# Optimization experiments

Hardware: AMD Instinct MI355X
Metric: run time of the kernel (lower is better)

Reference implementation:

```python
import jax, jax.numpy as jnp
import numpy as np

B, V, S = 128, 64, 40
D, H, VOC = 256, 256, 20000


def setup_inputs() -> dict:
    key = jax.random.key(0)
    ks = jax.random.split(key, 26)
    g = lambda k, shp: (jax.random.normal(k, shp, dtype=jnp.float32) * 0.02)
    inp = {}
    inp['input_seqs'] = jax.random.randint(ks[0], (B, V, S), 0, VOC + 1)
    inp['mask'] = jnp.zeros((B, V), jnp.float32)
    inp['length'] = jax.random.randint(ks[1], (B,), 1, V + 1)
    inp['seq_time_step'] = jax.random.uniform(ks[2], (B, V), dtype=jnp.float32)
    inp['codemask'] = jnp.zeros((B, V, S), jnp.float32)
    inp['label'] = jax.random.randint(ks[3], (B,), 0, 2)
    # embedding table; padding_idx=-1 in torch == row VOC zeroed
    inp['emb'] = g(ks[4], (VOC + 1, D)).at[VOC].set(0.0)
    # LSTM (single layer, batch_first): torch gate order i,f,g,o
    inp['W_ih'] = g(ks[5], (4 * H, D))
    inp['W_hh'] = g(ks[6], (4 * H, H))
    inp['b_ih'] = g(ks[7], (4 * H,))
    inp['b_hh'] = g(ks[8], (4 * H,))
    # attention projections
    inp['Whk'] = g(ks[9], (D, H))
    inp['bhk'] = g(ks[10], (D,))
    inp['W1'] = g(ks[11], (64, 2 * H))
    inp['b1'] = g(ks[12], (64,))
    inp['W2'] = g(ks[13], (2, 64))
    inp['b2'] = g(ks[14], (2,))
    # classifyer MLP: d -> 4d -> 2d -> 2
    inp['C1W'] = g(ks[15], (4 * D, D))
    inp['C1b'] = g(ks[16], (4 * D,))
    inp['C2W'] = g(ks[17], (2 * D, 4 * D))
    inp['C2b'] = g(ks[18], (2 * D,))
    inp['CoW'] = g(ks[19], (2, 2 * D))
    inp['Cob'] = g(ks[20], (2,))
    return inp


def _lstm(x, W_ih, W_hh, b_ih, b_hh):
    # x: [B,T,D] -> hs: [B,T,H]; torch gate order i,f,g,o
    Bsz = x.shape[0]
    Hd = W_hh.shape[1]
    xg = jnp.einsum('btd,gd->btg', x, W_ih) + b_ih + b_hh  # [B,T,4H]

    def step(carry, xg_t):
        h, c = carry
        gates = xg_t + h @ W_hh.T
        i, f, gg, o = jnp.split(gates, 4, axis=-1)
        i = jax.nn.sigmoid(i); f = jax.nn.sigmoid(f)
        gg = jnp.tanh(gg); o = jax.nn.sigmoid(o)
        c = f * c + i * gg
        h = o * jnp.tanh(c)
        return (h, c), h

    z = jnp.zeros((Bsz, Hd), x.dtype)
    _, hs = jax.lax.scan(step, (z, z), jnp.swapaxes(xg, 0, 1))
    return jnp.swapaxes(hs, 0, 1)


def _classify(h, C1W, C1b, C2W, C2b, CoW, Cob):
    h = jax.nn.relu(h @ C1W.T + C1b)
    h = jax.nn.relu(h @ C2W.T + C2b)
    return h @ CoW.T + Cob


def reference(input_seqs, mask, length, seq_time_step, codemask, label,
              emb, W_ih, W_hh, b_ih, b_hh, Whk, bhk, W1, b1, W2, b2,
              C1W, C1b, C2W, C2b, CoW, Cob):
    # before(): embedding gather -> relu -> sum over codes (eval mode, no dropout)
    v = jax.nn.relu(emb[input_seqs]).sum(-2)  # [B,V,D]
    h = _lstm(v, W_ih, W_hh, b_ih, b_hh)       # [B,V,H]

    # vectorized form of the per-timestep attention loop:
    # bar_v[:,0]=v[:,0]; for i>=1: mix of e_k=v[:,0] and w_hk(h[:,i-1])
    e_k = v[:, :1, :]                                   # [B,1,D]
    wh = h @ Whk.T + bhk                                # [B,V,D]
    wh_prev = wh[:, :-1, :]                             # [B,V-1,D] (h at i-1)
    e_b = jnp.broadcast_to(e_k, wh_prev.shape)
    cat = jnp.concatenate([e_b, wh_prev], axis=-1)      # [B,V-1,2D]
    attn = jax.nn.softmax(jnp.tanh(cat @ W1.T + b1) @ W2.T + b2, axis=-1)
    bar_rest = e_b * attn[..., 0:1] + wh_prev * attn[..., 1:2]
    bar_v = jnp.concatenate([v[:, :1, :], bar_rest], axis=1)  # [B,V,D]

    # GAN stand-in (external injected module): identity
    Dec_V, Gen_V = bar_v, bar_v
    gen_h = _lstm(Gen_V, W_ih, W_hh, b_ih, b_hh)

    og = _classify(h, C1W, C1b, C2W, C2b, CoW, Cob)        # [B,V,2]
    fake = _classify(gen_h, C1W, C1b, C2W, C2b, CoW, Cob)  # [B,V,2]
    final_og = og[:, -1, :]
    final_fake = fake[:, -1, :]
    return (final_og, final_fake, Dec_V, Gen_V, seq_time_step, label)
```

## Files before the change

kernel.cpp:

```cpp
#include <hip/hip_runtime.h>

#define DEV __device__ __forceinline__

typedef float f32x4 __attribute__((ext_vector_type(4)));
typedef short s16x8 __attribute__((ext_vector_type(8)));
typedef short s16x4 __attribute__((ext_vector_type(4)));

DEV unsigned short f2bf(float f){
  unsigned int u = __float_as_uint(f);
  u += 0x7fffu + ((u>>16)&1u);
  return (unsigned short)(u>>16);
}
DEV float bf2f(unsigned short h){ return __uint_as_float(((unsigned int)h)<<16); }

#if __has_builtin(__builtin_amdgcn_rcpf)
DEV float frcp_(float x){ return __builtin_amdgcn_rcpf(x); }
#else
DEV float frcp_(float x){ return 1.f/x; }
#endif
#if __has_builtin(__builtin_amdgcn_exp2f)
DEV float fexp2_(float x){ return __builtin_amdgcn_exp2f(x); }
#else
DEV float fexp2_(float x){ return exp2f(x); }
#endif

DEV float tanh_(float x){
  x = fminf(x, 30.f);
  float e = fexp2_(2.8853900817779268f*x);
  return (e-1.f)*frcp_(e+1.f);
}

DEV unsigned char f2e4m3(float x){
  unsigned int u = __float_as_uint(x);
  unsigned int s = (u>>24)&0x80u;
  unsigned int mag = u & 0x7fffffffu;
  if (mag > 0x43E00000u) mag = 0x43E00000u;
  mag += 0x000FFFFFu + ((mag>>20)&1u);
  int e = (int)(mag>>23) - 120;
  unsigned int m = (mag>>20)&7u;
  unsigned int r = (e<=0) ? 0u : (((unsigned)e<<3)|m);
  return (unsigned char)(s|r);
}

DEV f32x4 mfma_bf16(s16x8 a, s16x8 b, f32x4 c){
  return __builtin_amdgcn_mfma_f32_16x16x32_bf16(a,b,c,0,0,0);
}
DEV f32x4 mfma_fp8(long a, long b, f32x4 c){
  return __builtin_amdgcn_mfma_f32_16x16x32_fp8_fp8(a,b,c,0,0,0);
}

DEV void lds_barrier(){
  asm volatile("s_waitcnt lgkmcnt(0)\n\ts_barrier" ::: "memory");
}

DEV unsigned aload_rlx(unsigned* p){
  return __hip_atomic_load(p, __ATOMIC_RELAXED, __HIP_MEMORY_SCOPE_AGENT);
}
DEV void astore_rlx(unsigned* p, unsigned v){
  __hip_atomic_store(p, v, __ATOMIC_RELAXED, __HIP_MEMORY_SCOPE_AGENT);
}
DEV void aadd_rlx(unsigned* p, unsigned v){
  __hip_atomic_fetch_add(p, v, __ATOMIC_RELAXED, __HIP_MEMORY_SCOPE_AGENT);
}
DEV void acq_fence(){ __builtin_amdgcn_fence(__ATOMIC_ACQUIRE, "agent"); }
DEV void spin_rlx(unsigned* p, unsigned tgt){
  while (aload_rlx(p) < tgt) __builtin_amdgcn_s_sleep(2);
  asm volatile("" ::: "memory");
}
DEV void block_wait(unsigned* p, unsigned tgt){
  if (threadIdx.x == 0) spin_rlx(p, tgt);
  __syncthreads();
}
DEV void block_wait_acq(unsigned* p, unsigned tgt){
  if (threadIdx.x == 0){ spin_rlx(p, tgt); acq_fence(); }
  __syncthreads();
}
DEV s16x4 aload64(const unsigned short* p){
  unsigned long long v = __hip_atomic_load((unsigned long long*)(void*)p,
      __ATOMIC_RELAXED, __HIP_MEMORY_SCOPE_AGENT);
  union { unsigned long long u; s16x4 s; } c; c.u = v; return c.s;
}
DEV void astore64(unsigned short* p, s16x4 v){
  union { s16x4 s; unsigned long long u; } c; c.s = v;
  __hip_atomic_store((unsigned long long*)(void*)p, c.u,
      __ATOMIC_RELAXED, __HIP_MEMORY_SCOPE_AGENT);
}
DEV s16x8 aload128(const unsigned short* p){
  s16x4 a = aload64(p), b = aload64(p+4);
  s16x8 r;
  r[0]=a[0]; r[1]=a[1]; r[2]=a[2]; r[3]=a[3];
  r[4]=b[0]; r[5]=b[1]; r[6]=b[2]; r[7]=b[3];
  return r;
}
DEV float aloadf(const float* p){
  return __hip_atomic_load((float*)(void*)p, __ATOMIC_RELAXED, __HIP_MEMORY_SCOPE_AGENT);
}
DEV void astoref(float* p, float v){
  __hip_atomic_store(p, v, __ATOMIC_RELAXED, __HIP_MEMORY_SCOPE_AGENT);
}
DEV void astore16(unsigned short* p, unsigned short v){
  __hip_atomic_store(p, v, __ATOMIC_RELAXED, __HIP_MEMORY_SCOPE_AGENT);
}
DEV void vm_drain(){ asm volatile("s_waitcnt vmcnt(0)" ::: "memory"); }
DEV void ntf(float* p, float v){ __builtin_nontemporal_store(v, p); }

#define Bx 128
#define Vx 64
#define Sx 40
#define Dx 256
#define Hx 256
#define NVOC 20001

#define OFF_OG   0
#define OFF_FAKE 256
#define OFF_DECV 512
#define OFF_GENV 2097664
#define OFF_STS  4194816
#define OFF_LBL  4203008

#define PW_IH  0
#define PW_HH  262144
#define PW_HK  524288
#define PW_1   589824
#define PC_1   622592
#define PC_2   884736
#define PC_O   1409024
#define P_TOT  1410048

#define HPB 264
#define BFP 272
#define WHP 272

#define FCT(t)  ((t)*32)
#define FXG(t)  (2048 + (t)*32)
#define FUC     4096
#define FXG1(t) (4352 + (t)*32)
#define XDONE   6528
#define Y1D     6656
#define Y2D     6784
#define XG1A    6912
#define FTOT    8192

__global__ void k_cvt(const float* __restrict__ emb, unsigned short* __restrict__ emb16,
                      const float* __restrict__ W_ih, const float* __restrict__ Whh,
                      const float* __restrict__ Whk, const float* __restrict__ W1,
                      const float* __restrict__ C1W, const float* __restrict__ C2W,
                      const float* __restrict__ CoW,
                      unsigned short* __restrict__ pool, unsigned char* __restrict__ whh8,
                      const float* __restrict__ sts, const int* __restrict__ label,
                      float* __restrict__ out, unsigned* __restrict__ flags){
  int bx = blockIdx.x, tid = threadIdx.x;
  if (bx < NVOC){
    size_t i = (size_t)bx*256 + tid;
    emb16[i] = f2bf(emb[i]);
    return;
  }
  if (bx < NVOC + 6532){
    int i = (bx - NVOC)*256 + tid;
    if (i < P_TOT){
      float v;
      if      (i < PW_HH) v = W_ih[i - PW_IH];
      else if (i < PW_HK) v = Whh [i - PW_HH];
      else if (i < PW_1 ) v = Whk [i - PW_HK];
      else if (i < PC_1 ) v = W1  [i - PW_1 ];
      else if (i < PC_2 ) v = C1W [i - PC_1 ];
      else if (i < PC_O ) v = C2W [i - PC_2 ];
      else                v = CoW [i - PC_O ];
      pool[i] = f2bf(v);
    } else {
      whh8[i - P_TOT] = f2e4m3(16.f*Whh[i - P_TOT]);
    }
    return;
  }
  for (int i=tid;i<FTOT;i+=256) flags[i] = 0u;
  for (int i=tid;i<Bx*Vx;i+=256) out[OFF_STS + i] = sts[i];
  if (tid < Bx) out[OFF_LBL + tid] = (float)label[tid];
}

__global__ void k_pre2(const int* __restrict__ seqs, const unsigned short* __restrict__ emb16,
                       unsigned short* __restrict__ v16,
                       float* __restrict__ decv, float* __restrict__ genv){
  int bt = blockIdx.x, d = threadIdx.x;
  const int* sp = seqs + (size_t)bt*Sx;
  float acc = 0.f;
  #pragma unroll 8
  for (int s=0;s<Sx;s++) acc += fmaxf(bf2f(emb16[(size_t)sp[s]*Dx + d]), 0.f);
  size_t o = (size_t)bt*Dx + d;
  v16[o] = f2bf(acc);
  if ((bt & 63) == 0){ decv[o] = acc; genv[o] = acc; }
}

DEV void lstm_act(const f32x4* A, float* cst, float* hv){
  const float K1 = 1.4426950408889634f/256.f;
  #pragma unroll
  for (int r=0;r<4;r++){
    float iv = frcp_(1.f + fexp2_(-K1*A[0][r]));
    float fv = frcp_(1.f + fexp2_(-K1*A[1][r]));
    float eg = fexp2_(2.f*K1*A[2][r]);
    float gv = (eg-1.f)*frcp_(eg+1.f);
    float ov = frcp_(1.f + fexp2_(-K1*A[3][r]));
    float cv = fv*cst[r] + iv*gv;
    cst[r] = cv;
    float ec = fexp2_(2.8853900817779268f*fminf(cv,30.f));
    hv[r] = ov*(ec-1.f)*frcp_(ec+1.f);
  }
}

DEV void store_h_fp8(unsigned char* hn, int q, const float* hv){
#if __has_builtin(__builtin_amdgcn_cvt_pk_fp8_f32)
  int p01 = __builtin_amdgcn_cvt_pk_fp8_f32(16.f*hv[0], 16.f*hv[1], 0, false);
  int p23 = __builtin_amdgcn_cvt_pk_fp8_f32(16.f*hv[2], 16.f*hv[3], 0, false);
  hn[(q*4+0)*HPB] = (unsigned char)p01;
  hn[(q*4+1)*HPB] = (unsigned char)(p01>>8);
  hn[(q*4+2)*HPB] = (unsigned char)p23;
  hn[(q*4+3)*HPB] = (unsigned char)(p23>>8);
#else
  #pragma unroll
  for (int r=0;r<4;r++) hn[(q*4+r)*HPB] = f2e4m3(16.f*hv[r]);
#endif
}

DEV void scan1_body(unsigned char* smem, const unsigned char* __restrict__ W8,
                    const unsigned short* __restrict__ xg1, unsigned short* __restrict__ hist,
                    int g, unsigned* __restrict__ flags){
  unsigned char*  hl  = smem;
  unsigned short* h1b = (unsigned short*)(smem + 8448);
  int tid = threadIdx.x;
  int w = tid>>6, l = tid&63, lm = l&15, q = l>>4;
  int j = w*16 + lm;
  for (int i=tid;i<8448;i+=1024) hl[i] = 0;
  long Bf[4][8];
  #pragma unroll
  for (int qq=0;qq<4;qq++){
    int n = qq*256 + j;
    #pragma unroll
    for (int kk=0;kk<8;kk++)
      Bf[qq][kk] = *(const long*)(W8 + (size_t)n*256 + kk*32 + q*8);
  }
  float cst[4] = {0.f,0.f,0.f,0.f};
  const unsigned short* xgb = xg1 + (size_t)g*16384 + q*4;
  s16x4 xc[4], xn[4];
  block_wait(&flags[FXG1(0)], 2);
  #pragma unroll
  for (int qq=0;qq<4;qq++) xc[qq] = aload64(xgb + (qq*256+j)*16);
  int all1 = 0;
  const unsigned char* hrd = hl + lm*HPB + q*8;
  #pragma unroll 1
  for (int t=0;t<Vx;t++){
    if (t > 0){
      asm volatile("s_waitcnt vmcnt(0)" ::: "memory");
      __syncthreads();
    }
    if (tid == 0){
      if (t > 0) aadd_rlx(&flags[FCT(t-1)], 1);
      if (t < Vx-1 && !all1){
        spin_rlx(&flags[FXG1(t+1)], 2);
        all1 = (aload_rlx(&flags[XG1A]) >= 128);
      }
    }
    __syncthreads();
    if (t < Vx-1){
      #pragma unroll
      for (int qq=0;qq<4;qq++)
        xn[qq] = aload64(xgb + (size_t)(t+1)*131072 + (qq*256+j)*16);
    }
    const unsigned char* hb = hrd + (t&1)*4224;
    f32x4 A[4];
    #pragma unroll
    for (int qq=0;qq<4;qq++){
      #pragma unroll
      for (int r=0;r<4;r++) A[qq][r] = bf2f((unsigned short)xc[qq][r]);
    }
    #pragma unroll
    for (int kk=0;kk<8;kk++){
      long af = *(const long*)(hb + kk*32);
      A[0] = mfma_fp8(af, Bf[0][kk], A[0]);
      A[1] = mfma_fp8(af, Bf[1][kk], A[1]);
      A[2] = mfma_fp8(af, Bf[2][kk], A[2]);
      A[3] = mfma_fp8(af, Bf[3][kk], A[3]);
    }
    float hv[4];
    lstm_act(A, cst, hv);
    store_h_fp8(hl + ((t+1)&1)*4224 + j, q, hv);
    #pragma unroll
    for (int r=0;r<4;r++) h1b[(q*4+r)*BFP + j] = f2bf(hv[r]);
    lds_barrier();
    {
      int row = tid>>6, c4 = (tid&63)*4;
      s16x4 hx = *(const s16x4*)(h1b + row*BFP + c4);
      astore64(hist + ((size_t)t*Bx + g*16 + row)*Hx + c4, hx);
    }
    #pragma unroll
    for (int qq=0;qq<4;qq++) xc[qq] = xn[qq];
  }
  asm volatile("s_waitcnt vmcnt(0)" ::: "memory");
  __syncthreads();
  if (tid == 0){ aadd_rlx(&flags[FCT(63)], 1); aadd_rlx(&flags[XDONE], 1); }
}

DEV void scan2_body(unsigned char* smem, const unsigned char* __restrict__ W8,
                    const unsigned short* __restrict__ xg2, unsigned short* __restrict__ h2,
                    int g, unsigned* __restrict__ flags){
  unsigned char*  hl  = smem;
  unsigned short* h1b = (unsigned short*)(smem + 8448);
  int tid = threadIdx.x;
  int w = tid>>6, l = tid&63, lm = l&15, q = l>>4;
  int j = w*16 + lm;
  for (int i=tid;i<8448;i+=1024) hl[i] = 0;
  long Bf[4][8];
  #pragma unroll
  for (int qq=0;qq<4;qq++){
    int n = qq*256 + j;
    #pragma unroll
    for (int kk=0;kk<8;kk++)
      Bf[qq][kk] = *(const long*)(W8 + (size_t)n*256 + kk*32 + q*8);
  }
  float cst[4] = {0.f,0.f,0.f,0.f};
  const unsigned short* xgb = xg2 + (size_t)g*16384 + q*4;
  s16x4 xc[4], xn1[4], xn2[4];
  block_wait(&flags[FXG(0)], 1);
  #pragma unroll
  for (int qq=0;qq<4;qq++) xc[qq] = aload64(xgb + (qq*256+j)*16);
  block_wait(&flags[FXG(1)], 1);
  #pragma unroll
  for (int qq=0;qq<4;qq++) xn1[qq] = aload64(xgb + 131072 + (qq*256+j)*16);
  int skip = 0;
  const unsigned char* hrd = hl + lm*HPB + q*8;
  #pragma unroll 1
  for (int t=0;t<Vx;t++){
    if (t+2 < Vx){
      if (tid == 0){
        if (!skip) spin_rlx(&flags[FXG(t+2)], 1);
        skip = (t+3 < Vx) && (aload_rlx(&flags[FXG(t+3)]) >= 1);
      }
      __syncthreads();
      #pragma unroll
      for (int qq=0;qq<4;qq++)
        xn2[qq] = aload64(xgb + (size_t)(t+2)*131072 + (qq*256+j)*16);
    }
    const unsigned char* hb = hrd + (t&1)*4224;
    f32x4 A[4];
    #pragma unroll
    for (int qq=0;qq<4;qq++){
      #pragma unroll
      for (int r=0;r<4;r++) A[qq][r] = bf2f((unsigned short)xc[qq][r]);
    }
    #pragma unroll
    for (int kk=0;kk<8;kk++){
      long af = *(const long*)(hb + kk*32);
      A[0] = mfma_fp8(af, Bf[0][kk], A[0]);
      A[1] = mfma_fp8(af, Bf[1][kk], A[1]);
      A[2] = mfma_fp8(af, Bf[2][kk], A[2]);
      A[3] = mfma_fp8(af, Bf[3][kk], A[3]);
    }
    float hv[4];
    lstm_act(A, cst, hv);
    store_h_fp8(hl + ((t+1)&1)*4224 + j, q, hv);
    if (t == Vx-1){
      #pragma unroll
      for (int r=0;r<4;r++) h1b[(q*4+r)*BFP + j] = f2bf(hv[r]);
      lds_barrier();
      {
        int row = tid>>6, c4 = (tid&63)*4;
        s16x4 hx = *(const s16x4*)(h1b + row*BFP + c4);
        astore64(h2 + (size_t)(g*16 + row)*Hx + c4, hx);
      }
      asm volatile("s_waitcnt vmcnt(0)" ::: "memory");
      __syncthreads();
      if (tid == 0) aadd_rlx(&flags[XDONE], 1);
    } else {
      lds_barrier();
    }
    #pragma unroll
    for (int qq=0;qq<4;qq++){ xc[qq] = xn1[qq]; xn1[qq] = xn2[qq]; }
  }
}

template<int ALDS>
DEV void xg2_tile(const unsigned short* Ab, const unsigned short* __restrict__ pool,
                  const float* __restrict__ b_ih, const float* __restrict__ b_hh,
                  unsigned short* __restrict__ xg2, int tile, int w, int lm, int q){
  int mh = (w&1)*64, nb = (w>>1)*128;
  #pragma unroll 1
  for (int sc=0; sc<4; sc++){
    int n0 = nb + sc*32;
    f32x4 acc[4][2];
    #pragma unroll
    for (int nt=0;nt<2;nt++){
      int n = n0 + nt*16 + lm;
      float bz = b_ih[n] + b_hh[n];
      #pragma unroll
      for (int mt=0;mt<4;mt++) acc[mt][nt] = (f32x4){bz,bz,bz,bz};
    }
    #pragma unroll
    for (int kk=0;kk<8;kk++){
      s16x8 bfr[2];
      #pragma unroll
      for (int nt=0;nt<2;nt++){
        int n = n0 + nt*16 + lm;
        bfr[nt] = *(const s16x8*)(pool + PW_IH + (size_t)n*256 + kk*32 + q*8);
      }
      #pragma unroll
      for (int mt=0;mt<4;mt++){
        int row = mh + mt*16 + lm;
        s16x8 afr = ALDS ? *(const s16x8*)(Ab + (size_t)row*WHP + kk*32 + q*8)
                         : *(const s16x8*)(Ab + (size_t)row*Vx*Dx + kk*32 + q*8);
        acc[mt][0] = mfma_bf16(afr, bfr[0], acc[mt][0]);
        acc[mt][1] = mfma_bf16(afr, bfr[1], acc[mt][1]);
      }
    }
    #pragma unroll
    for (int mt=0;mt<4;mt++){
      int m = mh + mt*16 + q*4;
      int gg = m>>4;
      #pragma unroll
      for (int nt=0;nt<2;nt++){
        int n = n0 + nt*16 + lm;
        s16x4 sv;
        #pragma unroll
        for (int r=0;r<4;r++) sv[r] = (short)f2bf(256.f*acc[mt][nt][r]);
        astore64(xg2 + (((size_t)tile*8 + gg)*1024 + n)*16 + (m&15), sv);
      }
    }
  }
}

DEV void worker_body(unsigned short* whs, int t,
    const unsigned short* __restrict__ hist1, const unsigned short* __restrict__ v16,
    const float* __restrict__ u, const unsigned short* __restrict__ pool,
    const float* __restrict__ bhk, const float* __restrict__ W2, const float* __restrict__ b2,
    const float* __restrict__ b_ih, const float* __restrict__ b_hh,
    float* __restrict__ decv, float* __restrict__ genv,
    unsigned short* __restrict__ xg2, unsigned* __restrict__ flags){
  int tid = threadIdx.x, w = tid>>6, l = tid&63, lm = l&15, q = l>>4;
  if (t == 63){
    xg2_tile<0>(v16, pool, b_ih, b_hh, xg2, 0, w, lm, q);
    vm_drain();
    __syncthreads();
    if (tid == 0) astore_rlx(&flags[FXG(0)], 1);
    return;
  }
  block_wait(&flags[FCT(t)], 8);
  {
    int r0 = (w&7)*16, n0 = (w>>3)*128;
    const unsigned short* Ar = hist1 + ((size_t)t*Bx + r0 + lm)*Hx;
    f32x4 acc[8];
    #pragma unroll
    for (int nt=0;nt<8;nt++){
      float bz = bhk[n0 + nt*16 + lm];
      acc[nt] = (f32x4){bz,bz,bz,bz};
    }
    #pragma unroll
    for (int kk=0;kk<8;kk++){
      s16x8 afr = aload128(Ar + kk*32 + q*8);
      #pragma unroll
      for (int nt=0;nt<8;nt++){
        int n = n0 + nt*16 + lm;
        s16x8 bfr = *(const s16x8*)(pool + PW_HK + (size_t)n*256 + kk*32 + q*8);
        acc[nt] = mfma_bf16(afr, bfr, acc[nt]);
      }
    }
    #pragma unroll
    for (int nt=0;nt<8;nt++){
      int n = n0 + nt*16 + lm, mb = r0 + q*4;
      #pragma unroll
      for (int r=0;r<4;r++) whs[(size_t)(mb+r)*WHP + n] = f2bf(acc[nt][r]);
    }
  }
  if (tid == 0) spin_rlx(&flags[FUC], 8);
  __syncthreads();
  if (w < 8){
    int m0l = w*16;
    f32x4 a2[4];
    #pragma unroll
    for (int nt=0;nt<4;nt++){
      int n = nt*16 + lm;
      #pragma unroll
      for (int r=0;r<4;r++) a2[nt][r] = aloadf(u + (size_t)(m0l + q*4 + r)*64 + n);
    }
    #pragma unroll
    for (int kk=0;kk<8;kk++){
      s16x8 afr = *(const s16x8*)(whs + (size_t)(m0l+lm)*WHP + kk*32 + q*8);
      #pragma unroll
      for (int nt=0;nt<4;nt++){
        int n = nt*16 + lm;
        s16x8 bfr = *(const s16x8*)(pool + PW_1 + (size_t)n*512 + 256 + kk*32 + q*8);
        a2[nt] = mfma_bf16(afr, bfr, a2[nt]);
      }
    }
    float p0a[4] = {0,0,0,0}, p1a[4] = {0,0,0,0};
    #pragma unroll
    for (int nt=0;nt<4;nt++){
      int n = nt*16 + lm;
      float w2a = W2[n], w2b = W2[64+n];
      #pragma unroll
      for (int r=0;r<4;r++){
        float z = tanh_(a2[nt][r]);
        p0a[r] += z*w2a; p1a[r] += z*w2b;
      }
    }
    #pragma unroll
    for (int s=1;s<16;s<<=1){
      #pragma unroll
      for (int r=0;r<4;r++){ p0a[r] += __shfl_xor(p0a[r], s, 16); p1a[r] += __shfl_xor(p1a[r], s, 16); }
    }
    float bb0 = b2[0], bb1 = b2[1];
    int d0 = lm*16;
    #pragma unroll
    for (int r=0;r<4;r++){
      int b = m0l + q*4 + r;
      float g0 = p0a[r]+bb0, g1 = p1a[r]+bb1;
      float al0 = frcp_(1.f + fexp2_(1.4426950408889634f*(g1-g0)));
      float al1 = 1.f - al0;
      const unsigned short* ek = v16 + (size_t)b*Vx*Dx + d0;
      unsigned short* whp = whs + (size_t)b*WHP + d0;
      size_t ob = ((size_t)b*Vx + (t+1))*Dx + d0;
      #pragma unroll
      for (int c=0;c<2;c++){
        s16x8 e8 = *(const s16x8*)(ek + c*8);
        s16x8 w8 = *(const s16x8*)(whp + c*8);
        s16x8 o16;
        #pragma unroll
        for (int jj=0;jj<8;jj++){
          float o = al0*bf2f((unsigned short)e8[jj]) + al1*bf2f((unsigned short)w8[jj]);
          ntf(decv + ob + c*8 + jj, o);
          ntf(genv + ob + c*8 + jj, o);
          o16[jj] = (short)f2bf(o);
        }
        *(s16x8*)(whp + c*8) = o16;
      }
    }
  }
  __syncthreads();
  xg2_tile<1>(whs, pool, b_ih, b_hh, xg2, t+1, w, lm, q);
  vm_drain();
  __syncthreads();
  if (tid == 0) astore_rlx(&flags[FXG(t+1)], 1);
}

DEV void xg1_body(const unsigned short* __restrict__ v16, const unsigned short* __restrict__ pool,
                  const float* __restrict__ b_ih, const float* __restrict__ b_hh,
                  unsigned short* __restrict__ xg1, int blk, unsigned* __restrict__ flags){
  int tid = threadIdx.x, w = tid>>6, l = tid&63, lm = l&15, q = l>>4;
  int m0 = blk*64;
  int n0 = w*64;
  f32x4 acc[4][4];
  #pragma unroll
  for (int nt=0;nt<4;nt++){
    int n = n0 + nt*16 + lm;
    float bz = b_ih[n] + b_hh[n];
    #pragma unroll
    for (int mt=0;mt<4;mt++) acc[mt][nt] = (f32x4){bz,bz,bz,bz};
  }
  const s16x8* Arow[4];
  #pragma unroll
  for (int mt=0;mt<4;mt++){
    int m = m0 + mt*16 + lm;
    Arow[mt] = (const s16x8*)(v16 + ((size_t)(m&127)*Vx + (m>>7))*(size_t)Dx);
  }
  for (int kk=0; kk<8; kk++){
    s16x8 bfr[4];
    #pragma unroll
    for (int nt=0;nt<4;nt++){
      int n = n0 + nt*16 + lm;
      bfr[nt] = *(const s16x8*)(pool + PW_IH + (size_t)n*256 + kk*32 + q*8);
    }
    #pragma unroll
    for (int mt=0;mt<4;mt++){
      s16x8 afr = Arow[mt][kk*4 + q];
      #pragma unroll
      for (int nt=0;nt<4;nt++)
        acc[mt][nt] = mfma_bf16(afr, bfr[nt], acc[mt][nt]);
    }
  }
  #pragma unroll
  for (int mt=0;mt<4;mt++){
    int mbase = m0 + mt*16 + q*4;
    int tt = mbase>>7, bb = mbase&127;
    int gg = bb>>4;
    #pragma unroll
    for (int nt=0;nt<4;nt++){
      int n = n0 + nt*16 + lm;
      s16x4 sv;
      #pragma unroll
      for (int r=0;r<4;r++) sv[r] = (short)f2bf(256.f*acc[mt][nt][r]);
      astore64(xg1 + (((size_t)tt*8 + gg)*1024 + n)*16 + (bb&15), sv);
    }
  }
  vm_drain();
  __syncthreads();
  if (tid == 0){ aadd_rlx(&flags[FXG1(blk>>1)], 1); aadd_rlx(&flags[XG1A], 1); }
}

DEV void cls_gemm(const unsigned short* __restrict__ A, const unsigned short* __restrict__ Bw,
                  const float* __restrict__ bias, unsigned short* __restrict__ C,
                  int K, int Ntot, int bxx, int byy){
  int tid = threadIdx.x, w = tid>>6, l = tid&63, lm = l&15, q = l>>4;
  int m0 = bxx*64, n0 = byy*256 + w*64;
  f32x4 acc[4][4];
  #pragma unroll
  for (int nt=0;nt<4;nt++){
    int n = n0 + nt*16 + lm;
    float bz = bias[n];
    #pragma unroll
    for (int mt=0;mt<4;mt++) acc[mt][nt] = (f32x4){bz,bz,bz,bz};
  }
  const s16x8* Arow[4];
  #pragma unroll
  for (int mt=0;mt<4;mt++)
    Arow[mt] = (const s16x8*)(A + (size_t)(m0 + mt*16 + lm)*K);
  int kkn = K/32;
  for (int kk=0; kk<kkn; kk++){
    s16x8 bfr[4];
    #pragma unroll
    for (int nt=0;nt<4;nt++){
      int n = n0 + nt*16 + lm;
      bfr[nt] = *(const s16x8*)(Bw + (size_t)n*K + kk*32 + q*8);
    }
    #pragma unroll
    for (int mt=0;mt<4;mt++){
      s16x8 afr = Arow[mt][kk*4 + q];
      #pragma unroll
      for (int nt=0;nt<4;nt++)
        acc[mt][nt] = mfma_bf16(afr, bfr[nt], acc[mt][nt]);
    }
  }
  #pragma unroll
  for (int mt=0;mt<4;mt++){
    int mbase = m0 + mt*16 + q*4;
    #pragma unroll
    for (int nt=0;nt<4;nt++){
      int n = n0 + nt*16 + lm;
      #pragma unroll
      for (int r=0;r<4;r++)
        astore16(C + (size_t)(mbase+r)*Ntot + n, f2bf(fmaxf(acc[mt][nt][r], 0.f)));
    }
  }
}

__global__ __launch_bounds__(1024) void k_mega(
    const unsigned char* __restrict__ W8,
    unsigned short* __restrict__ xg1, unsigned short* __restrict__ xg2,
    unsigned short* __restrict__ hist1,
    const unsigned short* __restrict__ v16, float* __restrict__ u,
    const unsigned short* __restrict__ pool,
    const float* __restrict__ bhk, const float* __restrict__ W2, const float* __restrict__ b2,
    const float* __restrict__ b1, const float* __restrict__ b_ih, const float* __restrict__ b_hh,
    const float* __restrict__ C1b, const float* __restrict__ C2b, const float* __restrict__ Cob,
    float* __restrict__ decv, float* __restrict__ genv, float* __restrict__ out,
    unsigned* __restrict__ flags){
  __shared__ __align__(16) unsigned char smem[69632];
  int blk = blockIdx.x;
  unsigned short* X  = hist1 + (size_t)(Vx-1)*Bx*Hx;
  unsigned short* h2 = hist1 + (size_t)Vx*Bx*Hx;
  unsigned short* y1 = xg1;
  unsigned short* y2 = xg1 + 262144;
  if (blk < 8){
    scan1_body(smem, W8, xg1, hist1, blk, flags);
  } else if (blk < 16){
    scan2_body(smem, W8, xg2, h2, blk-8, flags);
  } else if (blk < 80){
    worker_body((unsigned short*)smem, blk-16, hist1, v16, u, pool, bhk, W2, b2,
                b_ih, b_hh, decv, genv, xg2, flags);
  } else if (blk < 88){
    int t2 = (blk-80)*1024 + threadIdx.x;
    int b = t2>>6, n = t2&63;
    const s16x8* vr = (const s16x8*)(v16 + (size_t)b*Vx*Dx);
    const s16x8* wr = (const s16x8*)(pool + PW_1 + (size_t)n*512);
    float a = b1[n];
    for (int kk=0;kk<32;kk++){
      s16x8 x = vr[kk], ww = wr[kk];
      #pragma unroll
      for (int jj=0;jj<8;jj++) a += bf2f((unsigned short)x[jj])*bf2f((unsigned short)ww[jj]);
    }
    astoref(u + t2, a);
    vm_drain();
    __syncthreads();
    if (threadIdx.x == 0) aadd_rlx(&flags[FUC], 1);
  } else if (blk < 216){
    xg1_body(v16, pool, b_ih, b_hh, xg1, blk-88, flags);
  } else if (blk < 232){
    block_wait_acq(&flags[XDONE], 16);
    int p = blk-216;
    if (threadIdx.x < 256) cls_gemm(X, pool+PC_1, C1b, y1, 256, 1024, p&3, p>>2);
    vm_drain();
    __syncthreads();
    if (threadIdx.x == 0) aadd_rlx(&flags[Y1D], 1);
  } else if (blk < 240){
    block_wait_acq(&flags[Y1D], 16);
    int p = blk-232;
    if (threadIdx.x < 256) cls_gemm(y1, pool+PC_2, C2b, y2, 1024, 512, p&3, p>>2);
    vm_drain();
    __syncthreads();
    if (threadIdx.x == 0) aadd_rlx(&flags[Y2D], 1);
  } else {
    block_wait_acq(&flags[Y2D], 8);
    if (threadIdx.x < 256){
      int t2 = (blk-240)*256 + threadIdx.x;
      int m = t2>>1, n = t2&1;
      const s16x8* yr = (const s16x8*)(y2 + (size_t)m*512);
      const s16x8* wr = (const s16x8*)(pool + PC_O + (size_t)n*512);
      float a = Cob[n];
      for (int kk=0;kk<64;kk++){
        s16x8 yv = yr[kk], ww = wr[kk];
        #pragma unroll
        for (int jj=0;jj<8;jj++) a += bf2f((unsigned short)yv[jj])*bf2f((unsigned short)ww[jj]);
      }
      int base = (m < 128) ? (OFF_OG + m*2) : (OFF_FAKE + (m-128)*2);
      out[base + n] = a;
    }
  }
}

extern "C" void kernel_launch(void* const* d_in, const int* in_sizes, int n_in,
                              void* d_out, int out_size, void* d_ws, size_t ws_size,
                              hipStream_t stream) {
  const int*   seqs  = (const int*)d_in[0];
  const float* sts   = (const float*)d_in[3];
  const int*   label = (const int*)d_in[5];
  const float* emb   = (const float*)d_in[6];
  const float* W_ih  = (const float*)d_in[7];
  const float* W_hh  = (const float*)d_in[8];
  const float* b_ih  = (const float*)d_in[9];
  const float* b_hh  = (const float*)d_in[10];
  const float* Whk   = (const float*)d_in[11];
  const float* bhk   = (const float*)d_in[12];
  const float* W1    = (const float*)d_in[13];
  const float* b1    = (const float*)d_in[14];
  const float* W2    = (const float*)d_in[15];
  const float* b2    = (const float*)d_in[16];
  const float* C1b   = (const float*)d_in[18];
  const float* C2b   = (const float*)d_in[20];
  const float* Cob   = (const float*)d_in[22];
  float* out = (float*)d_out;

  char* ws = (char*)d_ws;
  unsigned short* v16    = (unsigned short*)(ws + 0);
  unsigned short* xg1    = (unsigned short*)(ws + (4<<20));
  unsigned short* hist1  = (unsigned short*)(ws + (20<<20));
  unsigned short* xg2    = (unsigned short*)(ws + (25<<20));
  unsigned short* emb16  = xg2;
  float*          u      = (float*)(ws + (41<<20));
  unsigned char*  whh8   = (unsigned char*)(ws + (41<<20) + (64<<10));
  unsigned*       flags  = (unsigned*)(ws + (41<<20) + (384<<10));
  unsigned short* pool   = (unsigned short*)(ws + (42<<20));

  float* decv = out + OFF_DECV;
  float* genv = out + OFF_GENV;

  k_cvt<<<dim3(NVOC + 6532 + 1), dim3(256), 0, stream>>>(emb, emb16,
      W_ih, W_hh, Whk, W1, (const float*)d_in[17], (const float*)d_in[19],
      (const float*)d_in[21], pool, whh8, sts, label, out, flags);
  k_pre2<<<dim3(8192), dim3(256), 0, stream>>>(seqs, emb16, v16, decv, genv);
  k_mega<<<dim3(242), dim3(1024), 0, stream>>>(whh8, xg1, xg2, hist1, v16, u, pool,
      bhk, W2, b2, b1, b_ih, b_hh, C1b, C2b, Cob, decv, genv, out, flags);
}
```

Before: 508.9 us.

## Move input-gate GEMM to separate kernel and batch LSTM step flag signaling

The input-to-gate projection for the first LSTM now runs as its own kernel before the persistent mega-kernel, instead of as extra blocks inside it guarded by per-timestep flags. That lets the scan read xg1 with plain loads and no spin-waits. The scan now signals downstream consumers only every four timesteps, with a cheap LDS barrier in between. Conversion work is also regrouped into two kernels. The trade-off is an extra launch, losing the overlap between the GEMM and the scan, and coarser producer/consumer granularity for the workers that wait on FCT flags.

```diff
diff --git a/kernel.cpp b/kernel.cpp
--- a/kernel.cpp
+++ b/kernel.cpp
@@ -85,16 +85,6 @@
   __hip_atomic_store((unsigned long long*)(void*)p, c.u,
       __ATOMIC_RELAXED, __HIP_MEMORY_SCOPE_AGENT);
 }
-DEV s16x8 aload128(const unsigned short* p){
-  s16x4 a = aload64(p), b = aload64(p+4);
-  s16x8 r;
-  r[0]=a[0]; r[1]=a[1]; r[2]=a[2]; r[3]=a[3];
-  r[4]=b[0]; r[5]=b[1]; r[6]=b[2]; r[7]=b[3];
-  return r;
-}
-DEV float aloadf(const float* p){
-  return __hip_atomic_load((float*)(void*)p, __ATOMIC_RELAXED, __HIP_MEMORY_SCOPE_AGENT);
-}
 DEV void astoref(float* p, float v){
   __hip_atomic_store(p, v, __ATOMIC_RELAXED, __HIP_MEMORY_SCOPE_AGENT);
 }
@@ -134,14 +124,19 @@
 #define FCT(t)  ((t)*32)
 #define FXG(t)  (2048 + (t)*32)
 #define FUC     4096
-#define FXG1(t) (4352 + (t)*32)
-#define XDONE   6528
-#define Y1D     6656
-#define Y2D     6784
-#define XG1A    6912
+#define XDONE   4224
+#define Y1D     4352
+#define Y2D     4480
 #define FTOT    8192
 
-__global__ void k_cvt(const float* __restrict__ emb, unsigned short* __restrict__ emb16,
+__global__ void k_cvt_emb(const float* __restrict__ emb, unsigned short* __restrict__ emb16){
+  size_t i = (size_t)blockIdx.x*256 + threadIdx.x;
+  emb16[i] = f2bf(emb[i]);
+}
+
+__global__ void k_pre(const int* __restrict__ seqs, const unsigned short* __restrict__ emb16,
+                      unsigned short* __restrict__ v16,
+                      float* __restrict__ decv, float* __restrict__ genv,
                       const float* __restrict__ W_ih, const float* __restrict__ Whh,
                       const float* __restrict__ Whk, const float* __restrict__ W1,
                       const float* __restrict__ C1W, const float* __restrict__ C2W,
@@ -150,13 +145,19 @@
                       const float* __restrict__ sts, const int* __restrict__ label,
                       float* __restrict__ out, unsigned* __restrict__ flags){
   int bx = blockIdx.x, tid = threadIdx.x;
-  if (bx < NVOC){
-    size_t i = (size_t)bx*256 + tid;
-    emb16[i] = f2bf(emb[i]);
+  if (bx < 8192){
+    int bt = bx, d = tid;
+    const int* sp = seqs + (size_t)bt*Sx;
+    float acc = 0.f;
+    #pragma unroll 8
+    for (int s=0;s<Sx;s++) acc += fmaxf(bf2f(emb16[(size_t)sp[s]*Dx + d]), 0.f);
+    size_t o = (size_t)bt*Dx + d;
+    v16[o] = f2bf(acc);
+    if ((bt & 63) == 0){ decv[o] = acc; genv[o] = acc; }
     return;
   }
-  if (bx < NVOC + 6532){
-    int i = (bx - NVOC)*256 + tid;
+  if (bx < 14724){
+    int i = (bx-8192)*256 + tid;
     if (i < P_TOT){
       float v;
       if      (i < PW_HH) v = W_ih[i - PW_IH];
@@ -167,7 +168,7 @@
       else if (i < PC_O ) v = C2W [i - PC_2 ];
       else                v = CoW [i - PC_O ];
       pool[i] = f2bf(v);
-    } else {
+    } else if (i < P_TOT + 262144){
       whh8[i - P_TOT] = f2e4m3(16.f*Whh[i - P_TOT]);
     }
     return;
@@ -177,17 +178,68 @@
   if (tid < Bx) out[OFF_LBL + tid] = (float)label[tid];
 }
 
-__global__ void k_pre2(const int* __restrict__ seqs, const unsigned short* __restrict__ emb16,
-                       unsigned short* __restrict__ v16,
-                       float* __restrict__ decv, float* __restrict__ genv){
-  int bt = blockIdx.x, d = threadIdx.x;
-  const int* sp = seqs + (size_t)bt*Sx;
-  float acc = 0.f;
-  #pragma unroll 8
-  for (int s=0;s<Sx;s++) acc += fmaxf(bf2f(emb16[(size_t)sp[s]*Dx + d]), 0.f);
-  size_t o = (size_t)bt*Dx + d;
-  v16[o] = f2bf(acc);
-  if ((bt & 63) == 0){ decv[o] = acc; genv[o] = acc; }
+template<int MODE_A, int MODE_C, int RELU>
+__global__ void k_gemm(const unsigned short* __restrict__ A, const unsigned short* __restrict__ Bw,
+                       const float* __restrict__ bias1, const float* __restrict__ bias2,
+                       unsigned short* __restrict__ C, int K, int Ntot, float scale){
+  int tid = threadIdx.x, w = tid>>6, l = tid&63, lm = l&15, q = l>>4;
+  int m0 = blockIdx.x*64;
+  int n0 = blockIdx.y*256 + w*64;
+  f32x4 acc[4][4];
+  #pragma unroll
+  for (int nt=0;nt<4;nt++){
+    int n = n0 + nt*16 + lm;
+    float bz = bias1 ? bias1[n] : 0.f;
+    if (bias2) bz += bias2[n];
+    #pragma unroll
+    for (int mt=0;mt<4;mt++) acc[mt][nt] = (f32x4){bz,bz,bz,bz};
+  }
+  const s16x8* Arow[4];
+  #pragma unroll
+  for (int mt=0;mt<4;mt++){
+    int m = m0 + mt*16 + lm;
+    size_t off = (MODE_A==0) ? (size_t)m*K : ((size_t)(m&127)*Vx + (m>>7))*(size_t)K;
+    Arow[mt] = (const s16x8*)(A + off);
+  }
+  int kkn = K/32;
+  for (int kk=0; kk<kkn; kk++){
+    s16x8 bfr[4];
+    #pragma unroll
+    for (int nt=0;nt<4;nt++){
+      int n = n0 + nt*16 + lm;
+      bfr[nt] = *(const s16x8*)(Bw + (size_t)n*K + kk*32 + q*8);
+    }
+    #pragma unroll
+    for (int mt=0;mt<4;mt++){
+      s16x8 afr = Arow[mt][kk*4 + q];
+      #pragma unroll
+      for (int nt=0;nt<4;nt++)
+        acc[mt][nt] = mfma_bf16(afr, bfr[nt], acc[mt][nt]);
+    }
+  }
+  #pragma unroll
+  for (int mt=0;mt<4;mt++){
+    int mbase = m0 + mt*16 + q*4;
+    #pragma unroll
+    for (int nt=0;nt<4;nt++){
+      int n = n0 + nt*16 + lm;
+      if (MODE_C==0){
+        #pragma unroll
+        for (int r=0;r<4;r++){
+          float val = scale*acc[mt][nt][r];
+          if (RELU) val = fmaxf(val, 0.f);
+          C[(size_t)(mbase+r)*Ntot + n] = f2bf(val);
+        }
+      } else {
+        int tt = mbase>>7, bb = mbase&127;
+        int gg = bb>>4;
+        s16x4 sv;
+        #pragma unroll
+        for (int r=0;r<4;r++) sv[r] = (short)f2bf(scale*acc[mt][nt][r]);
+        *(s16x4*)(C + (((size_t)tt*8 + gg)*1024 + n)*16 + (bb&15)) = sv;
+      }
+    }
+  }
 }
 
 DEV void lstm_act(const f32x4* A, float* cst, float* hv){
@@ -240,29 +292,16 @@
   float cst[4] = {0.f,0.f,0.f,0.f};
   const unsigned short* xgb = xg1 + (size_t)g*16384 + q*4;
   s16x4 xc[4], xn[4];
-  block_wait(&flags[FXG1(0)], 2);
-  #pragma unroll
-  for (int qq=0;qq<4;qq++) xc[qq] = aload64(xgb + (qq*256+j)*16);
-  int all1 = 0;
+  #pragma unroll
+  for (int qq=0;qq<4;qq++) xc[qq] = *(const s16x4*)(xgb + (qq*256+j)*16);
+  __syncthreads();
   const unsigned char* hrd = hl + lm*HPB + q*8;
   #pragma unroll 1
   for (int t=0;t<Vx;t++){
-    if (t > 0){
-      asm volatile("s_waitcnt vmcnt(0)" ::: "memory");
-      __syncthreads();
-    }
-    if (tid == 0){
-      if (t > 0) aadd_rlx(&flags[FCT(t-1)], 1);
-      if (t < Vx-1 && !all1){
-        spin_rlx(&flags[FXG1(t+1)], 2);
-        all1 = (aload_rlx(&flags[XG1A]) >= 128);
-      }
-    }
-    __syncthreads();
     if (t < Vx-1){
       #pragma unroll
       for (int qq=0;qq<4;qq++)
-        xn[qq] = aload64(xgb + (size_t)(t+1)*131072 + (qq*256+j)*16);
+        xn[qq] = *(const s16x4*)(xgb + (size_t)(t+1)*131072 + (qq*256+j)*16);
     }
     const unsigned char* hb = hrd + (t&1)*4224;
     f32x4 A[4];
@@ -290,12 +329,22 @@
       s16x4 hx = *(const s16x4*)(h1b + row*BFP + c4);
       astore64(hist + ((size_t)t*Bx + g*16 + row)*Hx + c4, hx);
     }
+    if ((t&3) == 3){
+      vm_drain();
+      __syncthreads();
+      if (tid == 0){
+        aadd_rlx(&flags[FCT(t-3)], 1);
+        aadd_rlx(&flags[FCT(t-2)], 1);
+        aadd_rlx(&flags[FCT(t-1)], 1);
+        aadd_rlx(&flags[FCT(t  )], 1);
+      }
+    } else {
+      lds_barrier();
+    }
     #pragma unroll
     for (int qq=0;qq<4;qq++) xc[qq] = xn[qq];
   }
-  asm volatile("s_waitcnt vmcnt(0)" ::: "memory");
-  __syncthreads();
-  if (tid == 0){ aadd_rlx(&flags[FCT(63)], 1); aadd_rlx(&flags[XDONE], 1); }
+  if (tid == 0) aadd_rlx(&flags[XDONE], 1);
 }
 
 DEV void scan2_body(unsigned char* smem, const unsigned char* __restrict__ W8,
@@ -365,7 +414,7 @@
         s16x4 hx = *(const s16x4*)(h1b + row*BFP + c4);
         astore64(h2 + (size_t)(g*16 + row)*Hx + c4, hx);
       }
-      asm volatile("s_waitcnt vmcnt(0)" ::: "memory");
+      vm_drain();
       __syncthreads();
       if (tid == 0) aadd_rlx(&flags[XDONE], 1);
     } else {
@@ -452,7 +501,7 @@
     }
     #pragma unroll
     for (int kk=0;kk<8;kk++){
-      s16x8 afr = aload128(Ar + kk*32 + q*8);
+      s16x8 afr = *(const s16x8*)(Ar + kk*32 + q*8);
       #pragma unroll
       for (int nt=0;nt<8;nt++){
         int n = n0 + nt*16 + lm;
@@ -476,7 +525,7 @@
     for (int nt=0;nt<4;nt++){
       int n = nt*16 + lm;
       #pragma unroll
-      for (int r=0;r<4;r++) a2[nt][r] = aloadf(u + (size_t)(m0l + q*4 + r)*64 + n);
+      for (int r=0;r<4;r++) a2[nt][r] = u[(size_t)(m0l + q*4 + r)*64 + n];
     }
     #pragma unroll
     for (int kk=0;kk<8;kk++){
@@ -536,60 +585,6 @@
   vm_drain();
   __syncthreads();
   if (tid == 0) astore_rlx(&flags[FXG(t+1)], 1);
-}
-
-DEV void xg1_body(const unsigned short* __restrict__ v16, const unsigned short* __restrict__ pool,
-                  const float* __restrict__ b_ih, const float* __restrict__ b_hh,
-                  unsigned short* __restrict__ xg1, int blk, unsigned* __restrict__ flags){
-  int tid = threadIdx.x, w = tid>>6, l = tid&63, lm = l&15, q = l>>4;
-  int m0 = blk*64;
-  int n0 = w*64;
-  f32x4 acc[4][4];
-  #pragma unroll
-  for (int nt=0;nt<4;nt++){
-    int n = n0 + nt*16 + lm;
-    float bz = b_ih[n] + b_hh[n];
-    #pragma unroll
-    for (int mt=0;mt<4;mt++) acc[mt][nt] = (f32x4){bz,bz,bz,bz};
-  }
-  const s16x8* Arow[4];
-  #pragma unroll
-  for (int mt=0;mt<4;mt++){
-    int m = m0 + mt*16 + lm;
-    Arow[mt] = (const s16x8*)(v16 + ((size_t)(m&127)*Vx + (m>>7))*(size_t)Dx);
-  }
-  for (int kk=0; kk<8; kk++){
-    s16x8 bfr[4];
-    #pragma unroll
-    for (int nt=0;nt<4;nt++){
-      int n = n0 + nt*16 + lm;
-      bfr[nt] = *(const s16x8*)(pool + PW_IH + (size_t)n*256 + kk*32 + q*8);
-    }
-    #pragma unroll
-    for (int mt=0;mt<4;mt++){
-      s16x8 afr = Arow[mt][kk*4 + q];
-      #pragma unroll
-      for (int nt=0;nt<4;nt++)
-        acc[mt][nt] = mfma_bf16(afr, bfr[nt], acc[mt][nt]);
-    }
-  }
-  #pragma unroll
-  for (int mt=0;mt<4;mt++){
-    int mbase = m0 + mt*16 + q*4;
-    int tt = mbase>>7, bb = mbase&127;
-    int gg = bb>>4;
-    #pragma unroll
-    for (int nt=0;nt<4;nt++){
-      int n = n0 + nt*16 + lm;
-      s16x4 sv;
-      #pragma unroll
-      for (int r=0;r<4;r++) sv[r] = (short)f2bf(256.f*acc[mt][nt][r]);
-      astore64(xg1 + (((size_t)tt*8 + gg)*1024 + n)*16 + (bb&15), sv);
-    }
-  }
-  vm_drain();
-  __syncthreads();
-  if (tid == 0){ aadd_rlx(&flags[FXG1(blk>>1)], 1); aadd_rlx(&flags[XG1A], 1); }
 }
 
 DEV void cls_gemm(const unsigned short* __restrict__ A, const unsigned short* __restrict__ Bw,
@@ -677,18 +672,16 @@
     vm_drain();
     __syncthreads();
     if (threadIdx.x == 0) aadd_rlx(&flags[FUC], 1);
-  } else if (blk < 216){
-    xg1_body(v16, pool, b_ih, b_hh, xg1, blk-88, flags);
-  } else if (blk < 232){
+  } else if (blk < 104){
     block_wait_acq(&flags[XDONE], 16);
-    int p = blk-216;
+    int p = blk-88;
     if (threadIdx.x < 256) cls_gemm(X, pool+PC_1, C1b, y1, 256, 1024, p&3, p>>2);
     vm_drain();
     __syncthreads();
     if (threadIdx.x == 0) aadd_rlx(&flags[Y1D], 1);
-  } else if (blk < 240){
+  } else if (blk < 112){
     block_wait_acq(&flags[Y1D], 16);
-    int p = blk-232;
+    int p = blk-104;
     if (threadIdx.x < 256) cls_gemm(y1, pool+PC_2, C2b, y2, 1024, 512, p&3, p>>2);
     vm_drain();
     __syncthreads();
@@ -696,7 +689,7 @@
   } else {
     block_wait_acq(&flags[Y2D], 8);
     if (threadIdx.x < 256){
-      int t2 = (blk-240)*256 + threadIdx.x;
+      int t2 = (blk-112)*256 + threadIdx.x;
       int m = t2>>1, n = t2&1;
       const s16x8* yr = (const s16x8*)(y2 + (size_t)m*512);
       const s16x8* wr = (const s16x8*)(pool + PC_O + (size_t)n*512);
@@ -748,10 +741,11 @@
   float* decv = out + OFF_DECV;
   float* genv = out + OFF_GENV;
 
-  k_cvt<<<dim3(NVOC + 6532 + 1), dim3(256), 0, stream>>>(emb, emb16,
+  k_cvt_emb<<<dim3(NVOC), dim3(256), 0, stream>>>(emb, emb16);
+  k_pre<<<dim3(14725), dim3(256), 0, stream>>>(seqs, emb16, v16, decv, genv,
       W_ih, W_hh, Whk, W1, (const float*)d_in[17], (const float*)d_in[19],
       (const float*)d_in[21], pool, whh8, sts, label, out, flags);
-  k_pre2<<<dim3(8192), dim3(256), 0, stream>>>(seqs, emb16, v16, decv, genv);
-  k_mega<<<dim3(242), dim3(1024), 0, stream>>>(whh8, xg1, xg2, hist1, v16, u, pool,
+  k_gemm<1,1,0><<<dim3(128,4), dim3(256), 0, stream>>>(v16, pool+PW_IH, b_ih, b_hh, xg1, 256, 1024, 256.f);
+  k_mega<<<dim3(114), dim3(1024), 0, stream>>>(whh8, xg1, xg2, hist1, v16, u, pool,
       bhk, W2, b2, b1, b_ih, b_hh, C1b, C2b, Cob, decv, genv, out, flags);
 }
```

Result: faster. 498.9 us (-2.0%).
